# Kernel optimization log

Measured on AMD Instinct MI355X. Metric: run time of the kernel, lower is better.

## Reference

```python
import jax, jax.numpy as jnp
import numpy as np

# irreps_in = irreps_out = "32x0e + 16x1o"; irreps_edge = "1x0e + 1x1o"
N_SCAL, N_VEC = 32, 16
RADIAL_EMBED, HIDDEN = 64, 64
# FullyConnectedTensorProduct instructions (uvw), v == 1 since edge mults are 1:
#  P1: 0e x 0e -> 0e (32*32)   P2: 1o x 1o -> 0e (16*32)
#  P3: 0e x 1o -> 1o (32*16)   P4: 1o x 0e -> 1o (16*16)   P5: 1o x 1o -> 1o (16*16)
SPLITS = np.cumsum([0, 32 * 32, 16 * 32, 32 * 16, 16 * 16, 16 * 16])
W_NUMEL = int(SPLITS[-1])  # 2560
SILU_NORM = 1.6790425  # e3nn normalize2mom constant for silu
# path weights: alpha = ir_out.dim / sum(num_elements over paths into same output)
PW0 = (1.0 / (32.0 + 16.0)) ** 0.5          # scalar output paths
PW1 = (3.0 / (32.0 + 16.0 + 16.0)) ** 0.5   # vector output paths
INV_SQRT3 = 3.0 ** -0.5  # wigner_3j(0,1,1)/(1,0,1)/(1,1,0) magnitude
INV_SQRT6 = 6.0 ** -0.5  # wigner_3j(1,1,1) = eps_ijk / sqrt(6)
N_NODES, N_EDGES = 8192, 65536


def radial_net(e, W0, W1, W2):
    # e3nn FullyConnectedNet: x @ (W / sqrt(fan_in)), normalized silu between layers
    h = e
    for W in (W0, W1):
        h = jax.nn.silu(h @ (W / jnp.sqrt(jnp.float32(W.shape[0])))) * SILU_NORM
    return h @ (W2 / jnp.sqrt(jnp.float32(W2.shape[0])))


def setup_inputs() -> dict:
    key = jax.random.key(0)
    ks = jax.random.split(key, 9)
    edge_index = jax.random.randint(ks[0], (2, N_EDGES), 0, N_NODES)
    node_feat = jax.random.normal(ks[1], (N_NODES, N_SCAL + 3 * N_VEC), jnp.float32)
    edge_feat = jax.random.normal(ks[2], (N_EDGES, 4), jnp.float32)
    edge_embed = jax.random.normal(ks[3], (N_EDGES, RADIAL_EMBED), jnp.float32)
    W_fc0 = jax.random.normal(ks[4], (RADIAL_EMBED, HIDDEN), jnp.float32)
    W_fc1 = jax.random.normal(ks[5], (HIDDEN, HIDDEN), jnp.float32)
    W_fc2 = jax.random.normal(ks[6], (HIDDEN, W_NUMEL), jnp.float32)
    Wsc0 = jax.random.normal(ks[7], (N_SCAL, N_SCAL), jnp.float32)
    Wsc1 = jax.random.normal(ks[8], (N_VEC, N_VEC), jnp.float32)
    return dict(edge_index=edge_index, node_feat=node_feat, edge_feat=edge_feat,
                edge_embed=edge_embed, dim_size=N_NODES,
                W_fc0=W_fc0, W_fc1=W_fc1, W_fc2=W_fc2, Wsc0=Wsc0, Wsc1=Wsc1)


def reference(edge_index, node_feat, edge_feat, edge_embed, dim_size,
              W_fc0, W_fc1, W_fc2, Wsc0, Wsc1):
    src, dst = edge_index[0], edge_index[1]
    w = radial_net(edge_embed, W_fc0, W_fc1, W_fc2)  # [E, 2560]
    W1 = w[:, SPLITS[0]:SPLITS[1]].reshape(-1, 32, 32)
    W2 = w[:, SPLITS[1]:SPLITS[2]].reshape(-1, 16, 32)
    W3 = w[:, SPLITS[2]:SPLITS[3]].reshape(-1, 32, 16)
    W4 = w[:, SPLITS[3]:SPLITS[4]].reshape(-1, 16, 16)
    W5 = w[:, SPLITS[4]:SPLITS[5]].reshape(-1, 16, 16)
    xe = node_feat[src]                                    # gather [E, 80]
    x0 = xe[:, :N_SCAL]                                    # [E, 32]
    x1 = xe[:, N_SCAL:].reshape(-1, N_VEC, 3)              # [E, 16, 3]
    y0, y1 = edge_feat[:, 0], edge_feat[:, 1:4]            # [E], [E, 3]
    # scalar outputs
    dot = jnp.einsum('eui,ei->eu', x1, y1)
    out0 = PW0 * (jnp.einsum('euw,eu,e->ew', W1, x0, y0)
                  + INV_SQRT3 * jnp.einsum('euw,eu->ew', W2, dot))
    # vector outputs ((x cross y)_k = eps_ijk x_i y_j)
    cross = jnp.cross(x1, y1[:, None, :])
    out1 = PW1 * (INV_SQRT3 * jnp.einsum('euw,eu,ek->ewk', W3, x0, y1)
                  + INV_SQRT3 * jnp.einsum('euw,euk,e->ewk', W4, x1, y0)
                  + INV_SQRT6 * jnp.einsum('euw,euk->ewk', W5, cross))
    msg = jnp.concatenate([out0, out1.reshape(-1, 3 * N_VEC)], axis=1)  # [E, 80]
    agg = jax.ops.segment_sum(msg, dst, num_segments=dim_size)          # [N, 80]
    # self-connection: e3nn o3.Linear applied per irrep, / sqrt(fan_in)
    n0 = node_feat[:, :N_SCAL]
    n1 = node_feat[:, N_SCAL:].reshape(-1, N_VEC, 3)
    sc0 = n0 @ Wsc0 / jnp.sqrt(jnp.float32(N_SCAL))
    sc1 = jnp.einsum('nui,uv->nvi', n1, Wsc1) / jnp.sqrt(jnp.float32(N_VEC))
    sc = jnp.concatenate([sc0, sc1.reshape(-1, 3 * N_VEC)], axis=1)
    return agg + sc
```

## Files before the change

kernel.cpp:

```cpp
#include <hip/hip_runtime.h>

typedef unsigned short u16;
typedef __bf16 bf16x8 __attribute__((ext_vector_type(8)));
typedef float  f32x4  __attribute__((ext_vector_type(4)));

#define NEDGES 65536
#define NNODES 8192
#define EPB 64

#define PW0f       0.14433756729740643f
#define PW1f       0.21650635094610965f
#define INV_SQRT3f 0.5773502691896258f
#define INV_SQRT6f 0.4082482904638631f
#define SILU_NORMf 1.6790425f

#define WT2_OFF 0
#define WT0_OFF 163840
#define WT1_OFF 167936
#define WS_ELEMS 172032

#define OFF_CNT   344064
#define OFF_OFS   376832
#define OFF_CUR   409856
#define OFF_ELIST 442624
#define OFF_MSG   704768
#define WS_NEED   21676288

#define HSTR 72

__device__ __forceinline__ float silu_n(float z) {
    return SILU_NORMf * z / (1.0f + __expf(-z));
}
__device__ __forceinline__ u16 f2bf(float f) {
    return __builtin_bit_cast(u16, (__bf16)f);
}
__device__ __forceinline__ float bf2f(u16 u) {
    unsigned v = ((unsigned)u) << 16;
    return __builtin_bit_cast(float, v);
}
__device__ __forceinline__ bf16x8 ld_bf8(const u16* p) {
    return *reinterpret_cast<const bf16x8*>(p);
}
__device__ __forceinline__ bf16x8 cvt_bf8(const float* p) {
    float4 a = *reinterpret_cast<const float4*>(p);
    float4 b = *reinterpret_cast<const float4*>(p + 4);
    bf16x8 r;
    r[0]=(__bf16)a.x; r[1]=(__bf16)a.y; r[2]=(__bf16)a.z; r[3]=(__bf16)a.w;
    r[4]=(__bf16)b.x; r[5]=(__bf16)b.y; r[6]=(__bf16)b.z; r[7]=(__bf16)b.w;
    return r;
}
#define MFMA16(A,B,C) __builtin_amdgcn_mfma_f32_16x16x32_bf16(A,B,C,0,0,0)

__global__ void k_zero(int* __restrict__ cnt) {
    int i = blockIdx.x * 256 + threadIdx.x;
    if (i < NNODES) cnt[i] = 0;
}

__global__ void k_prep(const float* __restrict__ Wfc0,
                       const float* __restrict__ Wfc1,
                       const float* __restrict__ Wfc2,
                       const float* __restrict__ node_feat,
                       const float* __restrict__ Wsc0,
                       const float* __restrict__ Wsc1,
                       const int*   __restrict__ eidx,
                       u16* __restrict__ ws,
                       int* __restrict__ cnt,
                       float* __restrict__ out)
{
    const int bid = blockIdx.x;
    if (bid < 672) {
        int gid = bid * 256 + threadIdx.x;
        if (gid < 163840) {
            int k = gid / 2560;
            int j = gid - k * 2560;
            float s;
            if (j < 1024)      s = PW0f;
            else if (j < 1536) s = PW0f * INV_SQRT3f;
            else if (j < 2304) s = PW1f * INV_SQRT3f;
            else               s = PW1f * INV_SQRT6f;
            ws[WT2_OFF + j * 64 + k] = f2bf(Wfc2[gid] * (0.125f * s));
        } else if (gid < WT1_OFF) {
            int i = gid - WT0_OFF;
            int k = i >> 6, n = i & 63;
            ws[WT0_OFF + n * 64 + k] = f2bf(Wfc0[i] * 0.125f);
        } else if (gid < WS_ELEMS) {
            int i = gid - WT1_OFF;
            int k = i >> 6, n = i & 63;
            ws[WT1_OFF + n * 64 + k] = f2bf(Wfc1[i] * 0.125f);
        }
    } else if (bid < 3232) {
        int gid = (bid - 672) * 256 + threadIdx.x;
        if (gid >= NNODES * 80) return;
        int n = gid / 80;
        int s = gid - n * 80;
        const float* nf = node_feat + (size_t)n * 80;
        float r;
        if (s < 32) {
            float a = 0.f;
            #pragma unroll
            for (int u = 0; u < 32; ++u) a += nf[u] * Wsc0[u * 32 + s];
            r = a * 0.17677669529663687f;
        } else {
            int v = (s - 32) / 3;
            int k = (s - 32) - v * 3;
            float a = 0.f;
            #pragma unroll
            for (int u = 0; u < 16; ++u) a += nf[32 + u * 3 + k] * Wsc1[u * 16 + v];
            r = a * 0.25f;
        }
        out[gid] = r;
    } else {
        int e = (bid - 3232) * 256 + threadIdx.x;
        if (e < NEDGES) atomicAdd(&cnt[eidx[NEDGES + e]], 1);
    }
}

__global__ __launch_bounds__(1024) void k_scan(const int* __restrict__ cnt,
                                               int* __restrict__ ofs,
                                               int* __restrict__ cur)
{
    __shared__ int ps[1024];
    const int t = threadIdx.x;
    const int base = t * 8;
    int v[8]; int s = 0;
    #pragma unroll
    for (int i = 0; i < 8; ++i) { v[i] = cnt[base + i]; s += v[i]; }
    ps[t] = s;
    __syncthreads();
    int acc = s;
    for (int off = 1; off < 1024; off <<= 1) {
        int x = (t >= off) ? ps[t - off] : 0;
        __syncthreads();
        acc += x;
        ps[t] = acc;
        __syncthreads();
    }
    int run = acc - s;
    #pragma unroll
    for (int i = 0; i < 8; ++i) { ofs[base + i] = run; cur[base + i] = run; run += v[i]; }
    if (t == 1023) ofs[NNODES] = run;
}

__global__ void k_fill(const int* __restrict__ eidx,
                       int* __restrict__ cur,
                       int* __restrict__ elist)
{
    int e = blockIdx.x * 256 + threadIdx.x;
    int d = eidx[NEDGES + e];
    int pos = atomicAdd(&cur[d], 1);
    elist[pos] = e;
}

template<int TAIL>
__global__ __launch_bounds__(256, 3) void k_main(
    const int*   __restrict__ eidx,
    const float* __restrict__ node_feat,
    const float* __restrict__ edge_feat,
    const float* __restrict__ edge_embed,
    const u16*   __restrict__ ws,
    float*       __restrict__ msgbuf,
    float*       __restrict__ out)
{
    __shared__ __align__(16) char smem[40192];
    u16*   h1S   = (u16*)(smem);
    u16*   c12S  = (u16*)(smem + 9216);
    u16*   coefB = (u16*)(smem + 15360);
    int*   dstS  = (int*)(smem + 39936);
    u16*   h0S   = (u16*)(smem + 15360);
    float* msgS  = (float*)(smem + 9216);

    const int t    = threadIdx.x;
    const int lane = t & 63;
    const int l15  = lane & 15;
    const int lq   = lane >> 4;
    const int wid  = t >> 6;
    const int role = (wid + blockIdx.x) & 3;
    const int eg0  = blockIdx.x * EPB;

    const u16* WT2 = ws + WT2_OFF;
    const u16* WT0 = ws + WT0_OFF;
    const u16* WT1 = ws + WT1_OFF;

    {
        const float* erow = edge_embed + (size_t)(eg0 + wid * 16 + l15) * 64 + 8 * lq;
        bf16x8 eB0 = cvt_bf8(erow);
        bf16x8 eB1 = cvt_bf8(erow + 32);
        #pragma unroll
        for (int ntl = 0; ntl < 4; ++ntl) {
            const u16* a = WT0 + (ntl * 16 + l15) * 64 + 8 * lq;
            bf16x8 A0 = ld_bf8(a);
            bf16x8 A1 = ld_bf8(a + 32);
            f32x4 z = {0.f, 0.f, 0.f, 0.f};
            z = MFMA16(A0, eB0, z);
            f32x4 dd = MFMA16(A1, eB1, z);
            ushort4 pk;
            pk.x = f2bf(silu_n(dd[0]));
            pk.y = f2bf(silu_n(dd[1]));
            pk.z = f2bf(silu_n(dd[2]));
            pk.w = f2bf(silu_n(dd[3]));
            *(ushort4*)&h0S[(wid * 16 + l15) * HSTR + ntl * 16 + lq * 4] = pk;
        }
    }
    {
        const u16* hrow = h0S + (wid * 16 + l15) * HSTR + 8 * lq;
        bf16x8 hB0 = ld_bf8(hrow);
        bf16x8 hB1 = ld_bf8(hrow + 32);
        #pragma unroll
        for (int ntl = 0; ntl < 4; ++ntl) {
            const u16* a = WT1 + (ntl * 16 + l15) * 64 + 8 * lq;
            bf16x8 A0 = ld_bf8(a);
            bf16x8 A1 = ld_bf8(a + 32);
            f32x4 z = {0.f, 0.f, 0.f, 0.f};
            z = MFMA16(A0, hB0, z);
            f32x4 dd = MFMA16(A1, hB1, z);
            ushort4 pk;
            pk.x = f2bf(silu_n(dd[0]));
            pk.y = f2bf(silu_n(dd[1]));
            pk.z = f2bf(silu_n(dd[2]));
            pk.w = f2bf(silu_n(dd[3]));
            *(ushort4*)&h1S[(wid * 16 + l15) * HSTR + ntl * 16 + lq * 4] = pk;
        }
    }
    __syncthreads();

    {
        const int e   = t & 63;
        const int q   = t >> 6;
        const int eg  = eg0 + e;
        const int src = eidx[eg];
        const float* nf = node_feat + (size_t)src * 80;
        const float* ef = edge_feat + (size_t)eg * 4;
        if (q == 0) {
            dstS[e] = eidx[NEDGES + eg];
            const float y0 = ef[0];
            #pragma unroll
            for (int u = 0; u < 32; ++u) c12S[u * 64 + e] = f2bf(nf[u] * y0);
        } else if (q == 1) {
            const float ya = ef[1], yb = ef[2], yc = ef[3];
            #pragma unroll
            for (int u = 0; u < 16; ++u) {
                float d = nf[32 + u * 3] * ya + nf[32 + u * 3 + 1] * yb
                        + nf[32 + u * 3 + 2] * yc;
                c12S[(32 + u) * 64 + e] = f2bf(d);
            }
        } else if (q == 2) {
            const float ya = ef[1], yb = ef[2], yc = ef[3];
            #pragma unroll
            for (int u = 0; u < 32; ++u) {
                const float x = nf[u];
                coefB[(u * 3 + 0) * 64 + e] = f2bf(x * ya);
                coefB[(u * 3 + 1) * 64 + e] = f2bf(x * yb);
                coefB[(u * 3 + 2) * 64 + e] = f2bf(x * yc);
            }
        } else {
            const float y0 = ef[0], ya = ef[1], yb = ef[2], yc = ef[3];
            #pragma unroll
            for (int u = 0; u < 16; ++u) {
                const float xa = nf[32 + u * 3], xb = nf[32 + u * 3 + 1], xc = nf[32 + u * 3 + 2];
                coefB[(96 + u * 3 + 0) * 64 + e] = f2bf(xa * y0);
                coefB[(96 + u * 3 + 1) * 64 + e] = f2bf(xb * y0);
                coefB[(96 + u * 3 + 2) * 64 + e] = f2bf(xc * y0);
                coefB[(144 + u * 3 + 0) * 64 + e] = f2bf(xb * yc - xc * yb);
                coefB[(144 + u * 3 + 1) * 64 + e] = f2bf(xc * ya - xa * yc);
                coefB[(144 + u * 3 + 2) * 64 + e] = f2bf(xa * yb - xb * ya);
            }
        }
    }
    __syncthreads();

    bf16x8 hb[4][2];
    #pragma unroll
    for (int eg = 0; eg < 4; ++eg) {
        const u16* r = h1S + (eg * 16 + l15) * HSTR + 8 * lq;
        hb[eg][0] = ld_bf8(r);
        hb[eg][1] = ld_bf8(r + 32);
    }

    float acc[48];
    #pragma unroll
    for (int i = 0; i < 48; ++i) acc[i] = 0.f;

    int t0, ntile;
    if (role < 2) { t0 = role * 48;            ntile = 48; }
    else          { t0 = 96 + (role - 2) * 32; ntile = 32; }

    const u16* Aw = WT2 + l15 * 64 + 8 * lq;

#define COMPUTE(A0_, A1_, D_)                                          \
    {                                                                  \
        _Pragma("unroll")                                              \
        for (int eg = 0; eg < 4; ++eg) {                               \
            f32x4 z = {0.f, 0.f, 0.f, 0.f};                            \
            z = MFMA16(A0_, hb[eg][0], z);                             \
            D_[eg] = MFMA16(A1_, hb[eg][1], z);                        \
        }                                                              \
    }

#define EPILOGUE(D_, TT_, HS_)                                              \
    {                                                                       \
        if (role < 2) {                                                     \
            const u16* cr = c12S + ((TT_) >> 1) * 64;                       \
            _Pragma("unroll")                                               \
            for (int eg = 0; eg < 4; ++eg) {                                \
                const float c = bf2f(cr[eg * 16 + l15]);                    \
                _Pragma("unroll")                                           \
                for (int r = 0; r < 4; ++r)                                 \
                    acc[eg * 8 + (HS_) * 4 + r] += c * D_[eg][r];           \
            }                                                               \
        } else {                                                            \
            const u16* cr = coefB + ((TT_) - 96) * 192;                     \
            _Pragma("unroll")                                               \
            for (int eg = 0; eg < 4; ++eg) {                                \
                const int e16 = eg * 16 + l15;                              \
                const float c0 = bf2f(cr[e16]);                             \
                const float c1 = bf2f(cr[64 + e16]);                        \
                const float c2 = bf2f(cr[128 + e16]);                       \
                _Pragma("unroll")                                           \
                for (int r = 0; r < 4; ++r) {                               \
                    const float dv = D_[eg][r];                             \
                    acc[eg * 12 + r * 3 + 0] += c0 * dv;                    \
                    acc[eg * 12 + r * 3 + 1] += c1 * dv;                    \
                    acc[eg * 12 + r * 3 + 2] += c2 * dv;                    \
                }                                                           \
            }                                                               \
        }                                                                   \
    }

    bf16x8 Aa0, Aa1, Ab0, Ab1;
    {
        const u16* p = Aw + (size_t)t0 * 1024;
        Aa0 = ld_bf8(p); Aa1 = ld_bf8(p + 32);
        const u16* q = Aw + (size_t)(t0 + 1) * 1024;
        Ab0 = ld_bf8(q); Ab1 = ld_bf8(q + 32);
    }
    const int np = ntile >> 1;
    #pragma unroll 1
    for (int p = 0; p < np; ++p) {
        const int tt = t0 + 2 * p;
        bf16x8 Ac0, Ac1, Ad0, Ad1;
        const bool more = (p + 1 < np);
        if (more) {
            const u16* q = Aw + (size_t)(tt + 2) * 1024;
            Ac0 = ld_bf8(q); Ac1 = ld_bf8(q + 32);
        }
        f32x4 d[4];
        COMPUTE(Aa0, Aa1, d);
        EPILOGUE(d, tt, 0);
        if (more) {
            const u16* q = Aw + (size_t)(tt + 3) * 1024;
            Ad0 = ld_bf8(q); Ad1 = ld_bf8(q + 32);
        }
        COMPUTE(Ab0, Ab1, d);
        EPILOGUE(d, tt + 1, 1);
        if (more) { Aa0 = Ac0; Aa1 = Ac1; Ab0 = Ad0; Ab1 = Ad1; }
    }
#undef COMPUTE
#undef EPILOGUE

    __syncthreads();
    if (role == 0) {
        #pragma unroll
        for (int eg = 0; eg < 4; ++eg) {
            float* mb = msgS + (eg * 16 + l15) * 81;
            #pragma unroll
            for (int hs = 0; hs < 2; ++hs)
                #pragma unroll
                for (int r = 0; r < 4; ++r)
                    mb[hs * 16 + lq * 4 + r] = acc[eg * 8 + hs * 4 + r];
        }
    } else if (role == 2) {
        #pragma unroll
        for (int eg = 0; eg < 4; ++eg) {
            float* mb = msgS + (eg * 16 + l15) * 81 + 32;
            #pragma unroll
            for (int r = 0; r < 4; ++r)
                #pragma unroll
                for (int k = 0; k < 3; ++k)
                    mb[(lq * 4 + r) * 3 + k] = acc[eg * 12 + r * 3 + k];
        }
    }
    __syncthreads();
    if (role == 1) {
        #pragma unroll
        for (int eg = 0; eg < 4; ++eg) {
            float* mb = msgS + (eg * 16 + l15) * 81;
            #pragma unroll
            for (int hs = 0; hs < 2; ++hs)
                #pragma unroll
                for (int r = 0; r < 4; ++r)
                    mb[hs * 16 + lq * 4 + r] += acc[eg * 8 + hs * 4 + r];
        }
    } else if (role == 3) {
        #pragma unroll
        for (int eg = 0; eg < 4; ++eg) {
            float* mb = msgS + (eg * 16 + l15) * 81 + 32;
            #pragma unroll
            for (int r = 0; r < 4; ++r)
                #pragma unroll
                for (int k = 0; k < 3; ++k)
                    mb[(lq * 4 + r) * 3 + k] += acc[eg * 12 + r * 3 + k];
        }
    }
    __syncthreads();

    if (TAIL == 1) {
        float* mrow = msgbuf + (size_t)eg0 * 80;
        for (int idx = t; idx < EPB * 80; idx += 256) {
            const int e = idx / 80;
            const int s = idx - e * 80;
            mrow[idx] = msgS[e * 81 + s];
        }
    } else {
        for (int idx = t; idx < 64 * 81; idx += 256) {
            const int e = idx / 81;
            const int s = idx - e * 81;
            if (s < 80)
                atomicAdd(out + (size_t)dstS[e] * 80 + s, msgS[idx]);
        }
    }
}

__global__ __launch_bounds__(256) void k_gather(const int* __restrict__ ofs,
                                                const int* __restrict__ elist,
                                                const float* __restrict__ msg,
                                                float* __restrict__ out)
{
    const int lane = threadIdx.x & 63;
    const int n = blockIdx.x * 4 + (threadIdx.x >> 6);
    const int jb = ofs[n], je = ofs[n + 1];
    float v0 = 0.f, v1 = 0.f;
    int j = jb;
    for (; j + 2 <= je; j += 2) {
        const int e0 = elist[j], e1 = elist[j + 1];
        const float* m0 = msg + (size_t)e0 * 80;
        const float* m1 = msg + (size_t)e1 * 80;
        v0 += m0[lane] + m1[lane];
        if (lane < 16) v1 += m0[64 + lane] + m1[64 + lane];
    }
    if (j < je) {
        const float* m0 = msg + (size_t)elist[j] * 80;
        v0 += m0[lane];
        if (lane < 16) v1 += m0[64 + lane];
    }
    float* op = out + (size_t)n * 80;
    op[lane] += v0;
    if (lane < 16) op[64 + lane] += v1;
}

extern "C" void kernel_launch(void* const* d_in, const int* in_sizes, int n_in,
                              void* d_out, int out_size, void* d_ws, size_t ws_size,
                              hipStream_t stream) {
    const int*   eidx       = (const int*)d_in[0];
    const float* node_feat  = (const float*)d_in[1];
    const float* edge_feat  = (const float*)d_in[2];
    const float* edge_embed = (const float*)d_in[3];
    const float* Wfc0       = (const float*)d_in[5];
    const float* Wfc1       = (const float*)d_in[6];
    const float* Wfc2       = (const float*)d_in[7];
    const float* Wsc0       = (const float*)d_in[8];
    const float* Wsc1       = (const float*)d_in[9];
    float* out = (float*)d_out;
    char*  wsb = (char*)d_ws;
    u16*   ws  = (u16*)d_ws;

    if (ws_size < (size_t)WS_ELEMS * sizeof(u16)) return;

    const bool big = ws_size >= (size_t)WS_NEED;
    int*   cnt    = (int*)(wsb + OFF_CNT);
    int*   ofs    = (int*)(wsb + OFF_OFS);
    int*   cur    = (int*)(wsb + OFF_CUR);
    int*   elist  = (int*)(wsb + OFF_ELIST);
    float* msgbuf = (float*)(wsb + OFF_MSG);

    if (big) {
        hipLaunchKernelGGL(k_zero, dim3(32), dim3(256), 0, stream, cnt);
        hipLaunchKernelGGL(k_prep, dim3(3488), dim3(256), 0, stream,
                           Wfc0, Wfc1, Wfc2, node_feat, Wsc0, Wsc1, eidx, ws, cnt, out);
        hipLaunchKernelGGL(k_scan, dim3(1), dim3(1024), 0, stream, cnt, ofs, cur);
        hipLaunchKernelGGL(k_fill, dim3(NEDGES / 256), dim3(256), 0, stream,
                           eidx, cur, elist);
        hipLaunchKernelGGL((k_main<1>), dim3(NEDGES / EPB), dim3(256), 0, stream,
                           eidx, node_feat, edge_feat, edge_embed, ws, msgbuf, out);
        hipLaunchKernelGGL(k_gather, dim3(NNODES / 4), dim3(256), 0, stream,
                           ofs, elist, msgbuf, out);
    } else {
        hipLaunchKernelGGL(k_prep, dim3(3232), dim3(256), 0, stream,
                           Wfc0, Wfc1, Wfc2, node_feat, Wsc0, Wsc1, eidx, ws, cnt, out);
        hipLaunchKernelGGL((k_main<0>), dim3(NEDGES / EPB), dim3(256), 0, stream,
                           eidx, node_feat, edge_feat, edge_embed, ws, msgbuf, out);
    }
}
```

Before: 102.9 us.

## Split waves by edge half and output irrep, factor P3 cross term, write directly

```diff
diff --git a/kernel.cpp b/kernel.cpp
--- a/kernel.cpp
+++ b/kernel.cpp
@@ -152,7 +152,7 @@
 }
 
 template<int TAIL>
-__global__ __launch_bounds__(256, 3) void k_main(
+__global__ __launch_bounds__(256, 4) void k_main(
     const int*   __restrict__ eidx,
     const float* __restrict__ node_feat,
     const float* __restrict__ edge_feat,
@@ -161,20 +161,21 @@
     float*       __restrict__ msgbuf,
     float*       __restrict__ out)
 {
-    __shared__ __align__(16) char smem[40192];
-    u16*   h1S   = (u16*)(smem);
-    u16*   c12S  = (u16*)(smem + 9216);
-    u16*   coefB = (u16*)(smem + 15360);
-    int*   dstS  = (int*)(smem + 39936);
-    u16*   h0S   = (u16*)(smem + 15360);
-    float* msgS  = (float*)(smem + 9216);
+    __shared__ __align__(16) char smem[36864];
+    u16*   h1S  = (u16*)(smem);
+    u16*   c12S = (u16*)(smem + 9216);
+    u16*   x0S  = (u16*)(smem + 15360);
+    u16*   w4S  = (u16*)(smem + 19456);
+    u16*   w5S  = (u16*)(smem + 27648);
+    float* y1S  = (float*)(smem + 35840);
+    int*   dstS = (int*)(smem + 36608);
+    u16*   h0S  = (u16*)(smem + 9216);
 
     const int t    = threadIdx.x;
     const int lane = t & 63;
     const int l15  = lane & 15;
     const int lq   = lane >> 4;
     const int wid  = t >> 6;
-    const int role = (wid + blockIdx.x) & 3;
     const int eg0  = blockIdx.x * EPB;
 
     const u16* WT2 = ws + WT2_OFF;
@@ -233,6 +234,7 @@
         if (q == 0) {
             dstS[e] = eidx[NEDGES + eg];
             const float y0 = ef[0];
+            y1S[e] = ef[1]; y1S[64 + e] = ef[2]; y1S[128 + e] = ef[3];
             #pragma unroll
             for (int u = 0; u < 32; ++u) c12S[u * 64 + e] = f2bf(nf[u] * y0);
         } else if (q == 1) {
@@ -243,87 +245,105 @@
                         + nf[32 + u * 3 + 2] * yc;
                 c12S[(32 + u) * 64 + e] = f2bf(d);
             }
+            #pragma unroll
+            for (int u = 0; u < 32; ++u) x0S[u * 64 + e] = f2bf(nf[u]);
         } else if (q == 2) {
+            const float y0 = ef[0];
+            #pragma unroll
+            for (int u = 0; u < 16; ++u) {
+                ushort4 pk;
+                pk.x = f2bf(nf[32 + u * 3 + 0] * y0);
+                pk.y = f2bf(nf[32 + u * 3 + 1] * y0);
+                pk.z = f2bf(nf[32 + u * 3 + 2] * y0);
+                pk.w = 0;
+                *(ushort4*)&w4S[(u * 64 + e) * 4] = pk;
+            }
+        } else {
             const float ya = ef[1], yb = ef[2], yc = ef[3];
-            #pragma unroll
-            for (int u = 0; u < 32; ++u) {
-                const float x = nf[u];
-                coefB[(u * 3 + 0) * 64 + e] = f2bf(x * ya);
-                coefB[(u * 3 + 1) * 64 + e] = f2bf(x * yb);
-                coefB[(u * 3 + 2) * 64 + e] = f2bf(x * yc);
-            }
-        } else {
-            const float y0 = ef[0], ya = ef[1], yb = ef[2], yc = ef[3];
             #pragma unroll
             for (int u = 0; u < 16; ++u) {
                 const float xa = nf[32 + u * 3], xb = nf[32 + u * 3 + 1], xc = nf[32 + u * 3 + 2];
-                coefB[(96 + u * 3 + 0) * 64 + e] = f2bf(xa * y0);
-                coefB[(96 + u * 3 + 1) * 64 + e] = f2bf(xb * y0);
-                coefB[(96 + u * 3 + 2) * 64 + e] = f2bf(xc * y0);
-                coefB[(144 + u * 3 + 0) * 64 + e] = f2bf(xb * yc - xc * yb);
-                coefB[(144 + u * 3 + 1) * 64 + e] = f2bf(xc * ya - xa * yc);
-                coefB[(144 + u * 3 + 2) * 64 + e] = f2bf(xa * yb - xb * ya);
+                ushort4 pk;
+                pk.x = f2bf(xb * yc - xc * yb);
+                pk.y = f2bf(xc * ya - xa * yc);
+                pk.z = f2bf(xa * yb - xb * ya);
+                pk.w = 0;
+                *(ushort4*)&w5S[(u * 64 + e) * 4] = pk;
             }
         }
     }
     __syncthreads();
 
-    bf16x8 hb[4][2];
+    const int wid2   = (wid + blockIdx.x) & 3;
+    const int egbase = (wid2 & 1) * 2;
+    const int S      = wid2 >> 1;
+
+    bf16x8 hb[2][2];
     #pragma unroll
-    for (int eg = 0; eg < 4; ++eg) {
-        const u16* r = h1S + (eg * 16 + l15) * HSTR + 8 * lq;
+    for (int eg = 0; eg < 2; ++eg) {
+        const u16* r = h1S + ((egbase + eg) * 16 + l15) * HSTR + 8 * lq;
         hb[eg][0] = ld_bf8(r);
         hb[eg][1] = ld_bf8(r + 32);
     }
 
-    float acc[48];
+    float acc[32];
     #pragma unroll
-    for (int i = 0; i < 48; ++i) acc[i] = 0.f;
-
-    int t0, ntile;
-    if (role < 2) { t0 = role * 48;            ntile = 48; }
-    else          { t0 = 96 + (role - 2) * 32; ntile = 32; }
+    for (int i = 0; i < 32; ++i) acc[i] = 0.f;
+
+    const int t0    = S ? 96 : 0;
+    const int ntile = S ? 64 : 96;
 
     const u16* Aw = WT2 + l15 * 64 + 8 * lq;
 
 #define COMPUTE(A0_, A1_, D_)                                          \
     {                                                                  \
         _Pragma("unroll")                                              \
-        for (int eg = 0; eg < 4; ++eg) {                               \
+        for (int eg = 0; eg < 2; ++eg) {                               \
             f32x4 z = {0.f, 0.f, 0.f, 0.f};                            \
             z = MFMA16(A0_, hb[eg][0], z);                             \
             D_[eg] = MFMA16(A1_, hb[eg][1], z);                        \
         }                                                              \
     }
 
-#define EPILOGUE(D_, TT_, HS_)                                              \
-    {                                                                       \
-        if (role < 2) {                                                     \
-            const u16* cr = c12S + ((TT_) >> 1) * 64;                       \
-            _Pragma("unroll")                                               \
-            for (int eg = 0; eg < 4; ++eg) {                                \
-                const float c = bf2f(cr[eg * 16 + l15]);                    \
-                _Pragma("unroll")                                           \
-                for (int r = 0; r < 4; ++r)                                 \
-                    acc[eg * 8 + (HS_) * 4 + r] += c * D_[eg][r];           \
-            }                                                               \
-        } else {                                                            \
-            const u16* cr = coefB + ((TT_) - 96) * 192;                     \
-            _Pragma("unroll")                                               \
-            for (int eg = 0; eg < 4; ++eg) {                                \
-                const int e16 = eg * 16 + l15;                              \
-                const float c0 = bf2f(cr[e16]);                             \
-                const float c1 = bf2f(cr[64 + e16]);                        \
-                const float c2 = bf2f(cr[128 + e16]);                       \
-                _Pragma("unroll")                                           \
-                for (int r = 0; r < 4; ++r) {                               \
-                    const float dv = D_[eg][r];                             \
-                    acc[eg * 12 + r * 3 + 0] += c0 * dv;                    \
-                    acc[eg * 12 + r * 3 + 1] += c1 * dv;                    \
-                    acc[eg * 12 + r * 3 + 2] += c2 * dv;                    \
-                }                                                           \
-            }                                                               \
-        }                                                                   \
+#define EPILOGUE(D_, TT_, HS_)                                               \
+    {                                                                        \
+        if (S == 0) {                                     \
+            const u16* cr = c12S + ((TT_) >> 1) * 64;                        \
+            _Pragma("unroll")                                                \
+            for (int eg = 0; eg < 2; ++eg) {                                 \
+                const float c = bf2f(cr[(egbase + eg) * 16 + l15]);          \
+                _Pragma("unroll")                                            \
+                for (int r = 0; r < 4; ++r)                                  \
+                    acc[eg * 8 + (HS_) * 4 + r] += c * D_[eg][r];            \
+            }                                                                \
+        } else if ((TT_) < 128) {             \
+            const u16* cr = x0S + ((TT_) - 96) * 64;                         \
+            _Pragma("unroll")                                                \
+            for (int eg = 0; eg < 2; ++eg) {                                 \
+                const float c = bf2f(cr[(egbase + eg) * 16 + l15]);          \
+                _Pragma("unroll")                                            \
+                for (int r = 0; r < 4; ++r)                                  \
+                    acc[24 + eg * 4 + r] += c * D_[eg][r];                   \
+            }                                                                \
+        } else {                                   \
+            const u16* cr = ((TT_) < 144 ? w4S + ((TT_) - 128) * 256         \
+                                         : w5S + ((TT_) - 144) * 256);       \
+            _Pragma("unroll")                                                \
+            for (int eg = 0; eg < 2; ++eg) {                                 \
+                const ushort4 cw =                                           \
+                    *(const ushort4*)&cr[((egbase + eg) * 16 + l15) * 4];    \
+                const float c0 = bf2f(cw.x);                                 \
+                const float c1 = bf2f(cw.y);                                 \
+                const float c2 = bf2f(cw.z);                                 \
+                _Pragma("unroll")                                            \
+                for (int r = 0; r < 4; ++r) {                                \
+                    const float dv = D_[eg][r];                              \
+                    acc[eg * 12 + r * 3 + 0] += c0 * dv;                     \
+                    acc[eg * 12 + r * 3 + 1] += c1 * dv;                     \
+                    acc[eg * 12 + r * 3 + 2] += c2 * dv;                     \
+                }                                                            \
+            }                                                                \
+        }                                                                    \
     }
 
     bf16x8 Aa0, Aa1, Ab0, Ab1;
@@ -343,7 +363,7 @@
             const u16* q = Aw + (size_t)(tt + 2) * 1024;
             Ac0 = ld_bf8(q); Ac1 = ld_bf8(q + 32);
         }
-        f32x4 d[4];
+        f32x4 d[2];
         COMPUTE(Aa0, Aa1, d);
         EPILOGUE(d, tt, 0);
         if (more) {
@@ -357,65 +377,67 @@
 #undef COMPUTE
 #undef EPILOGUE
 
-    __syncthreads();
-    if (role == 0) {
-        #pragma unroll
-        for (int eg = 0; eg < 4; ++eg) {
-            float* mb = msgS + (eg * 16 + l15) * 81;
-            #pragma unroll
-            for (int hs = 0; hs < 2; ++hs)
+    if (TAIL == 1) {
+        if (S == 0) {
+            #pragma unroll
+            for (int eg = 0; eg < 2; ++eg) {
+                const int e = (egbase + eg) * 16 + l15;
+                float* mb = msgbuf + (size_t)(eg0 + e) * 80 + lq * 4;
+                float4 v0, v1;
+                v0.x = acc[eg*8+0]; v0.y = acc[eg*8+1]; v0.z = acc[eg*8+2]; v0.w = acc[eg*8+3];
+                v1.x = acc[eg*8+4]; v1.y = acc[eg*8+5]; v1.z = acc[eg*8+6]; v1.w = acc[eg*8+7];
+                *(float4*)(mb)      = v0;
+                *(float4*)(mb + 16) = v1;
+            }
+        } else {
+            #pragma unroll
+            for (int eg = 0; eg < 2; ++eg) {
+                const int e = (egbase + eg) * 16 + l15;
+                const float wx = y1S[e], wy = y1S[64 + e], wz = y1S[128 + e];
+                float v[12];
                 #pragma unroll
-                for (int r = 0; r < 4; ++r)
-                    mb[hs * 16 + lq * 4 + r] = acc[eg * 8 + hs * 4 + r];
-        }
-    } else if (role == 2) {
-        #pragma unroll
-        for (int eg = 0; eg < 4; ++eg) {
-            float* mb = msgS + (eg * 16 + l15) * 81 + 32;
-            #pragma unroll
-            for (int r = 0; r < 4; ++r)
+                for (int r = 0; r < 4; ++r) {
+                    const float s = acc[24 + eg * 4 + r];
+                    v[r*3+0] = acc[eg*12 + r*3+0] + s * wx;
+                    v[r*3+1] = acc[eg*12 + r*3+1] + s * wy;
+                    v[r*3+2] = acc[eg*12 + r*3+2] + s * wz;
+                }
+                float* mb = msgbuf + (size_t)(eg0 + e) * 80 + 32 + lq * 12;
+                float4 a0, a1, a2;
+                a0.x=v[0]; a0.y=v[1]; a0.z=v[2];  a0.w=v[3];
+                a1.x=v[4]; a1.y=v[5]; a1.z=v[6];  a1.w=v[7];
+                a2.x=v[8]; a2.y=v[9]; a2.z=v[10]; a2.w=v[11];
+                *(float4*)(mb)     = a0;
+                *(float4*)(mb + 4) = a1;
+                *(float4*)(mb + 8) = a2;
+            }
+        }
+    } else {
+        if (S == 0) {
+            #pragma unroll
+            for (int eg = 0; eg < 2; ++eg) {
+                const int e = (egbase + eg) * 16 + l15;
+                float* ob = out + (size_t)dstS[e] * 80 + lq * 4;
                 #pragma unroll
-                for (int k = 0; k < 3; ++k)
-                    mb[(lq * 4 + r) * 3 + k] = acc[eg * 12 + r * 3 + k];
-        }
-    }
-    __syncthreads();
-    if (role == 1) {
-        #pragma unroll
-        for (int eg = 0; eg < 4; ++eg) {
-            float* mb = msgS + (eg * 16 + l15) * 81;
-            #pragma unroll
-            for (int hs = 0; hs < 2; ++hs)
+                for (int hs = 0; hs < 2; ++hs)
+                    #pragma unroll
+                    for (int r = 0; r < 4; ++r)
+                        atomicAdd(ob + hs * 16 + r, acc[eg * 8 + hs * 4 + r]);
+            }
+        } else {
+            #pragma unroll
+            for (int eg = 0; eg < 2; ++eg) {
+                const int e = (egbase + eg) * 16 + l15;
+                const float wx = y1S[e], wy = y1S[64 + e], wz = y1S[128 + e];
+                float* ob = out + (size_t)dstS[e] * 80 + 32 + lq * 12;
                 #pragma unroll
-                for (int r = 0; r < 4; ++r)
-                    mb[hs * 16 + lq * 4 + r] += acc[eg * 8 + hs * 4 + r];
-        }
-    } else if (role == 3) {
-        #pragma unroll
-        for (int eg = 0; eg < 4; ++eg) {
-            float* mb = msgS + (eg * 16 + l15) * 81 + 32;
-            #pragma unroll
-            for (int r = 0; r < 4; ++r)
-                #pragma unroll
-                for (int k = 0; k < 3; ++k)
-                    mb[(lq * 4 + r) * 3 + k] += acc[eg * 12 + r * 3 + k];
-        }
-    }
-    __syncthreads();
-
-    if (TAIL == 1) {
-        float* mrow = msgbuf + (size_t)eg0 * 80;
-        for (int idx = t; idx < EPB * 80; idx += 256) {
-            const int e = idx / 80;
-            const int s = idx - e * 80;
-            mrow[idx] = msgS[e * 81 + s];
-        }
-    } else {
-        for (int idx = t; idx < 64 * 81; idx += 256) {
-            const int e = idx / 81;
-            const int s = idx - e * 81;
-            if (s < 80)
-                atomicAdd(out + (size_t)dstS[e] * 80 + s, msgS[idx]);
+                for (int r = 0; r < 4; ++r) {
+                    const float s = acc[24 + eg * 4 + r];
+                    atomicAdd(ob + r*3+0, acc[eg*12 + r*3+0] + s * wx);
+                    atomicAdd(ob + r*3+1, acc[eg*12 + r*3+1] + s * wy);
+                    atomicAdd(ob + r*3+2, acc[eg*12 + r*3+2] + s * wz);
+                }
+            }
         }
     }
 }
```

Result: slower. 131.0 us (+27.2%).
